# Optimization experiments

Hardware: AMD Instinct MI355X
Metric: run time of the kernel (lower is better)

Reference implementation:

```python
import jax, jax.numpy as jnp
import numpy as np
from jax import lax

B, T, IN_DIM, HID, K_WIN, N_TAGS, N_LAYERS = 128, 1024, 42, 256, 11, 8, 5
PAD = K_WIN // 2


def conv1d(x, w, b, pad):
    # x: (B, C_in, T), w: (C_out, C_in, K) -> (B, C_out, T)
    out = lax.conv_general_dilated(x, w, (1,), [(pad, pad)],
                                   dimension_numbers=('NCH', 'OIH', 'NCH'))
    return out + b[None, :, None]


def setup_inputs() -> dict:
    key = jax.random.key(0)
    ks = jax.random.split(key, 20)
    inp = {}
    inp['x'] = jax.random.normal(ks[0], (B, T, IN_DIM), dtype=jnp.float32)
    inp['lengths'] = jnp.full((B,), T, dtype=jnp.int32)
    inp['mask'] = jnp.ones((B, T), dtype=bool)
    inp['tags'] = jax.random.randint(ks[1], (B, T), 0, N_TAGS).astype(jnp.int32)
    prev = IN_DIM
    for i in range(N_LAYERS):
        scale = 1.0 / np.sqrt(prev * K_WIN)
        inp[f'w{i}'] = jax.random.uniform(ks[2 + i], (HID, prev, K_WIN), minval=-scale, maxval=scale, dtype=jnp.float32)
        inp[f'b{i}'] = jax.random.uniform(ks[8 + i], (HID,), minval=-scale, maxval=scale, dtype=jnp.float32)
        prev = HID
    scale = 1.0 / np.sqrt(HID)
    inp['w_out'] = jax.random.uniform(ks[14], (N_TAGS, HID, 1), minval=-scale, maxval=scale, dtype=jnp.float32)
    inp['b_out'] = jax.random.uniform(ks[15], (N_TAGS,), minval=-scale, maxval=scale, dtype=jnp.float32)
    # torchcrf initializes transitions uniform(-0.1, 0.1)
    inp['start_trans'] = jax.random.uniform(ks[16], (N_TAGS,), minval=-0.1, maxval=0.1, dtype=jnp.float32)
    inp['end_trans'] = jax.random.uniform(ks[17], (N_TAGS,), minval=-0.1, maxval=0.1, dtype=jnp.float32)
    inp['trans'] = jax.random.uniform(ks[18], (N_TAGS, N_TAGS), minval=-0.1, maxval=0.1, dtype=jnp.float32)
    return inp


def _emissions(x, ws, bs, w_out, b_out):
    h = jnp.transpose(x, (0, 2, 1))  # (B, C, T)
    for w, b in zip(ws, bs):
        h = jnp.tanh(conv1d(h, w, b, PAD))
    em = conv1d(h, w_out, b_out, 0)  # (B, K, T)
    return jnp.transpose(em, (0, 2, 1))  # (B, T, K)


def _crf_nll(emissions, tags, mask, start_trans, end_trans, trans):
    # loss = -sum_b log p(tags_b | emissions_b); torchcrf reduction='sum'
    Bn = emissions.shape[0]
    maskf = mask.astype(emissions.dtype)
    idx_b = jnp.arange(Bn)
    # --- numerator: path score of gold tags ---
    score0 = start_trans[tags[:, 0]] + emissions[idx_b, 0, tags[:, 0]]
    em_rest = jnp.transpose(emissions[:, 1:], (1, 0, 2))   # (T-1, B, K)
    tag_rest = tags[:, 1:].T                                # (T-1, B)
    m_rest = maskf[:, 1:].T                                 # (T-1, B)

    def num_step(carry, inp):
        score, prev_tag = carry
        em_t, tag_t, m_t = inp
        step = trans[prev_tag, tag_t] + em_t[idx_b, tag_t]
        score = score + step * m_t
        prev_tag = jnp.where(m_t > 0, tag_t, prev_tag)
        return (score, prev_tag), None

    (score, last_tag), _ = lax.scan(num_step, (score0, tags[:, 0]), (em_rest, tag_rest, m_rest))
    score = score + end_trans[last_tag]
    # --- denominator: forward algorithm (log partition) ---
    alpha0 = start_trans[None, :] + emissions[:, 0]  # (B, K)

    def den_step(alpha, inp):
        em_t, m_t = inp
        nxt = jax.nn.logsumexp(alpha[:, :, None] + trans[None, :, :] + em_t[:, None, :], axis=1)
        return jnp.where(m_t[:, None] > 0, nxt, alpha), None

    alpha, _ = lax.scan(den_step, alpha0, (em_rest, m_rest))
    log_z = jax.nn.logsumexp(alpha + end_trans[None, :], axis=1)
    return -jnp.sum(score - log_z)


def reference(x, lengths, mask, tags, w0, b0, w1, b1, w2, b2, w3, b3, w4, b4,
              w_out, b_out, start_trans, end_trans, trans):
    em = _emissions(x, [w0, w1, w2, w3, w4], [b0, b1, b2, b3, b4], w_out, b_out)
    return _crf_nll(em, tags, mask, start_trans, end_trans, trans)
```

## Files before the change

kernel.cpp:

```cpp
#include <hip/hip_runtime.h>


#define B_ 128
#define T_ 1024
#define IN_DIM_ 42
#define HID_ 256
#define KW_ 11
#define NTAGS_ 8
#define SEG_ 32
#define SEGL_ (T_ / SEG_)

typedef __bf16 bf16x8 __attribute__((ext_vector_type(8)));
typedef float f32x4 __attribute__((ext_vector_type(4)));
typedef short s16x8 __attribute__((ext_vector_type(8)));
typedef int i32x4 __attribute__((ext_vector_type(4)));
typedef int i32x8 __attribute__((ext_vector_type(8)));

struct i4pair { i32x4 lo, hi; };
__device__ __forceinline__ i32x8 mk8(i32x4 lo, i32x4 hi) {
    i4pair p{lo, hi};
    return __builtin_bit_cast(i32x8, p);
}

__device__ __forceinline__ unsigned short f2bf(float f) {
    unsigned u = __builtin_bit_cast(unsigned, f);
    u += 0x7FFFu + ((u >> 16) & 1u);
    return (unsigned short)(u >> 16);
}
__device__ __forceinline__ float fast_tanh(float x) {
    float e = __expf(2.f * x);
    return 1.f - 2.f / (e + 1.f);
}
__device__ __forceinline__ unsigned char f2fp8(float v) {
    return (unsigned char)(__builtin_amdgcn_cvt_pk_fp8_f32(v, v, 0, false) & 0xff);
}

#define SZ0_ (KW_ * 2 * 16 * 512)
#define SZF8_ (22 * 16 * 64 * 32)

__global__ void pack_l0(const float* __restrict__ w0, unsigned short* __restrict__ wp) {
    for (int idx = blockIdx.x * 256 + threadIdx.x; idx < SZ0_;
         idx += gridDim.x * 256) {
        int it2 = idx >> 13;
        int cic = it2 & 1, k = it2 >> 1;
        int e    = idx & 7;
        int lane = (idx >> 3) & 63;
        int coc  = (idx >> 9) & 15;
        int co = coc * 16 + (lane & 15);
        int ci = cic * 32 + ((lane >> 4) & 3) * 8 + e;
        float v = (ci < IN_DIM_) ? w0[(co * IN_DIM_ + ci) * KW_ + k] : 0.f;
        wp[idx] = f2bf(v);
    }
}

__global__ void pack_f8(const float* __restrict__ w1, const float* __restrict__ w2,
                        const float* __restrict__ w3, const float* __restrict__ w4,
                        unsigned char* __restrict__ wp8) {
    const int total = 4 * SZF8_;
    for (int idx = blockIdx.x * 256 + threadIdx.x; idx < total;
         idx += gridDim.x * 256) {
        int L   = idx / SZF8_;
        int loc = idx - L * SZF8_;
        const float* w = (L == 0) ? w1 : (L == 1) ? w2 : (L == 2) ? w3 : w4;
        int e    = loc & 31;
        int lane = (loc >> 5) & 63;
        int coc  = (loc >> 11) & 15;
        int it   = loc >> 15;
        int cic  = it / KW_;
        int k    = it - cic * KW_;
        int co = coc * 16 + (lane & 15);
        int ci = cic * 128 + (lane >> 4) * 32 + e;
        wp8[idx] = f2fp8(256.f * w[(co * HID_ + ci) * KW_ + k]);
    }
}

__global__ __launch_bounds__(512, 4)
void conv_first(const float* __restrict__ x, const unsigned short* __restrict__ wpack,
                const float* __restrict__ bias, unsigned char* __restrict__ out) {
    constexpr int CIN = 64, ROWS = 138;
    __shared__ unsigned short lds[ROWS * CIN];

    const int tid  = threadIdx.x;
    const int wave = tid >> 6;
    const int lane = tid & 63;
    const int l15  = lane & 15;
    const int lhi  = lane >> 4;
    const int wr   = wave >> 2;
    const int wc   = wave & 3;
    const int b    = blockIdx.x >> 3;
    const int t0   = (blockIdx.x & 7) * 128;

    for (int u = tid; u < ROWS * 32; u += 512) {
        int r = u >> 5, m = u & 31;
        int gt = t0 - 5 + r;
        unsigned val = 0;
        if (gt >= 0 && gt < T_ && 2 * m < IN_DIM_) {
            float2 f = *(const float2*)&x[((size_t)b * T_ + gt) * IN_DIM_ + 2 * m];
            val = (unsigned)f2bf(f.x) | ((unsigned)f2bf(f.y) << 16);
        }
        int c = m >> 2;
        int p = c ^ ((r + 3) & 7);
        ((unsigned*)lds)[(r * CIN + p * 8) / 2 + (m & 3)] = val;
    }
    __syncthreads();

    f32x4 acc[4][4];
#pragma unroll
    for (int tf = 0; tf < 4; ++tf)
#pragma unroll
        for (int n = 0; n < 4; ++n) acc[tf][n] = (f32x4){0.f, 0.f, 0.f, 0.f};

    const unsigned short* wpq = wpack + (size_t)(wc * 4) * 512 + lane * 8;
    const int arow = (wr * 64 + l15) * CIN;
    const int l153 = l15 + 3;

    s16x8 Bq[2][4];
#pragma unroll
    for (int n = 0; n < 4; ++n) Bq[0][n] = *(const s16x8*)&wpq[n * 512];

#pragma unroll
    for (int k = 0; k < KW_; ++k) {
#pragma unroll
        for (int cic = 0; cic < 2; ++cic) {
            const int it2 = k * 2 + cic;
            const int nxt = it2 + 1;
#pragma unroll
            for (int n = 0; n < 4; ++n)
                Bq[nxt & 1][n] = *(const s16x8*)&wpq[(size_t)nxt * 8192 + n * 512];
            const int key = (l153 + k) & 7;
            const int ao  = arow + (((cic * 4 + lhi) ^ key) << 3);
            s16x8 a0 = *(const s16x8*)&lds[ao + (0 * 16 + k) * CIN];
            s16x8 a1 = *(const s16x8*)&lds[ao + (1 * 16 + k) * CIN];
            s16x8 a2 = *(const s16x8*)&lds[ao + (2 * 16 + k) * CIN];
            s16x8 a3 = *(const s16x8*)&lds[ao + (3 * 16 + k) * CIN];
            __builtin_amdgcn_s_setprio(1);
#pragma unroll
            for (int n = 0; n < 4; ++n) {
                bf16x8 bb = __builtin_bit_cast(bf16x8, Bq[it2 & 1][n]);
                acc[0][n] = __builtin_amdgcn_mfma_f32_16x16x32_bf16(
                    __builtin_bit_cast(bf16x8, a0), bb, acc[0][n], 0, 0, 0);
                acc[1][n] = __builtin_amdgcn_mfma_f32_16x16x32_bf16(
                    __builtin_bit_cast(bf16x8, a1), bb, acc[1][n], 0, 0, 0);
                acc[2][n] = __builtin_amdgcn_mfma_f32_16x16x32_bf16(
                    __builtin_bit_cast(bf16x8, a2), bb, acc[2][n], 0, 0, 0);
                acc[3][n] = __builtin_amdgcn_mfma_f32_16x16x32_bf16(
                    __builtin_bit_cast(bf16x8, a3), bb, acc[3][n], 0, 0, 0);
            }
            __builtin_amdgcn_s_setprio(0);
        }
    }

#pragma unroll
    for (int n = 0; n < 4; ++n) {
        int co = wc * 64 + n * 16 + l15;
        float bv = bias[co];
        int cch = co >> 4, cby = co & 15;
#pragma unroll
        for (int tf = 0; tf < 4; ++tf) {
#pragma unroll
            for (int r4 = 0; r4 < 4; ++r4) {
                int t = t0 + wr * 64 + tf * 16 + lhi * 4 + r4;
                float v = fast_tanh(acc[tf][n][r4] + bv);
                out[((size_t)b * T_ + t) * 256 + ((cch ^ (t & 15)) << 4) + cby] =
                    f2fp8(v);
            }
        }
    }
}

template <bool LAST>
__global__ __launch_bounds__(256, 3)
void conv_mid(const unsigned char* __restrict__ Hin,
              const unsigned char* __restrict__ wpack,
              const float* __restrict__ bias, unsigned char* __restrict__ out,
              const float* __restrict__ w_out, float* __restrict__ emout) {
    extern __shared__ unsigned char lds8[];

    const int tid  = threadIdx.x;
    const int wave = tid >> 6;
    const int lane = tid & 63;
    const int l15  = lane & 15;
    const int lhi  = lane >> 4;
    const int wc   = wave;
    const int b    = blockIdx.x >> 4;
    const int t0   = (blockIdx.x & 15) * 64;

    for (int c = wave; c < 19; c += 4) {
        int r0 = c * 4;
        int r  = r0 + (lane >> 4);
        int gt = t0 - 5 + r;
        gt = gt < 0 ? 0 : (gt >= T_ ? T_ - 1 : gt);
        const unsigned char* src =
            Hin + ((size_t)b * T_ + gt) * 256 + (lane & 15) * 16;
        __builtin_amdgcn_global_load_lds(
            (const __attribute__((address_space(1))) void*)src,
            (__attribute__((address_space(3))) void*)&lds8[r0 * 256], 16, 0, 0);
    }
    __syncthreads();
    if (t0 == 0) {
        for (int u = tid; u < 320; u += 256)
            ((unsigned*)lds8)[u] = 0;
    }
    if (t0 == T_ - 64) {
        for (int u = tid; u < 320; u += 256)
            ((unsigned*)&lds8[69 * 256])[u] = 0;
    }
    __syncthreads();

    f32x4 acc[4][4];
#pragma unroll
    for (int tf = 0; tf < 4; ++tf)
#pragma unroll
        for (int n = 0; n < 4; ++n) acc[tf][n] = (f32x4){0.f, 0.f, 0.f, 0.f};

    const unsigned char* wpB = wpack + (size_t)(wc * 4) * 2048 + lane * 32;

    i32x8 Aa[4], Bq[4];

#define LOAD_B(n_, itv)                                                        \
    {                                                                          \
        const unsigned char* p_ = wpB + (size_t)(itv) * 32768 + (n_) * 2048;   \
        Bq[n_] = mk8(*(const i32x4*)p_, *(const i32x4*)(p_ + 16));             \
    }

#pragma unroll
    for (int n = 0; n < 4; ++n) LOAD_B(n, 0);

#pragma unroll 1
    for (int kk = 0; kk < 22; ++kk) {
        const int cic_ = kk / KW_;
        const int kn_  = kk - cic_ * KW_;
        const int key_ = (l15 + kn_ + 11) & 15;
        const int ca_  = ((cic_ * 8 + lhi * 2) ^ key_) << 4;
        const int rb_  = (l15 + kn_) * 256 + ca_;
#pragma unroll
        for (int tf = 0; tf < 4; ++tf)
            Aa[tf] = mk8(*(const i32x4*)&lds8[rb_ + tf * 4096],
                         *(const i32x4*)&lds8[(rb_ + tf * 4096) ^ 16]);
#pragma unroll
        for (int n = 0; n < 4; ++n) {
            __builtin_amdgcn_s_setprio(1);
#pragma unroll
            for (int tf = 0; tf < 4; ++tf)
                acc[tf][n] = __builtin_amdgcn_mfma_scale_f32_16x16x128_f8f6f4(
                    Aa[tf], Bq[n], acc[tf][n], 0, 0,
                    0, 0x7F7F7F7F, 0, 0x7F7F7F7F);
            __builtin_amdgcn_s_setprio(0);
            LOAD_B(n, kk + 1);
        }
    }
#undef LOAD_B

    constexpr float INV = 1.f / 256.f;
    if constexpr (!LAST) {
#pragma unroll
        for (int n = 0; n < 4; ++n) {
            int co = wc * 64 + n * 16 + l15;
            float bv = bias[co];
            int cch = co >> 4, cby = co & 15;
#pragma unroll
            for (int tf = 0; tf < 4; ++tf) {
#pragma unroll
                for (int r4 = 0; r4 < 4; ++r4) {
                    int t = t0 + tf * 16 + lhi * 4 + r4;
                    float v = fast_tanh(acc[tf][n][r4] * INV + bv);
                    out[((size_t)b * T_ + t) * 256 + ((cch ^ (t & 15)) << 4) + cby] =
                        f2fp8(v);
                }
            }
        }
    } else {
        float wv[4][NTAGS_], bvn[4];
#pragma unroll
        for (int n = 0; n < 4; ++n) {
            int co = wc * 64 + n * 16 + l15;
            bvn[n] = bias[co];
#pragma unroll
            for (int tg = 0; tg < NTAGS_; ++tg) wv[n][tg] = w_out[tg * HID_ + co];
        }
        __syncthreads();
        float* pbuf = (float*)lds8;
#pragma unroll
        for (int tf = 0; tf < 4; ++tf) {
#pragma unroll
            for (int r4 = 0; r4 < 4; ++r4) {
                float h[4];
#pragma unroll
                for (int n = 0; n < 4; ++n)
                    h[n] = fast_tanh(acc[tf][n][r4] * INV + bvn[n]);
                float pt[NTAGS_];
#pragma unroll
                for (int tg = 0; tg < NTAGS_; ++tg)
                    pt[tg] = h[0] * wv[0][tg] + h[1] * wv[1][tg] +
                             h[2] * wv[2][tg] + h[3] * wv[3][tg];
#pragma unroll
                for (int off = 8; off; off >>= 1)
#pragma unroll
                    for (int tg = 0; tg < NTAGS_; ++tg)
                        pt[tg] += __shfl_down(pt[tg], off);
                if (l15 == 0) {
                    int tloc = tf * 16 + lhi * 4 + r4;
                    f32x4 lo = {pt[0], pt[1], pt[2], pt[3]};
                    f32x4 hi = {pt[4], pt[5], pt[6], pt[7]};
                    *(f32x4*)&pbuf[(wc * 64 + tloc) * 8]     = lo;
                    *(f32x4*)&pbuf[(wc * 64 + tloc) * 8 + 4] = hi;
                }
            }
        }
        __syncthreads();
        for (int u = tid; u < 64 * NTAGS_; u += 256) {
            float s = pbuf[u] + pbuf[512 + u] + pbuf[1024 + u] + pbuf[1536 + u];
            emout[((size_t)b * T_ + t0) * NTAGS_ + u] = s;
        }
    }
}

__global__ __launch_bounds__(256)
void crf_seg_kernel(const float* __restrict__ em, const float* __restrict__ tr,
                    const float* __restrict__ bo, float* __restrict__ segM) {
    const int gw   = blockIdx.x * 4 + (threadIdx.x >> 6);
    const int b    = gw >> 5;
    const int s    = gw & 31;
    const int lane = threadIdx.x & 63;
    const int i    = lane >> 3;
    const int j    = lane & 7;
    const float* emb = em + (size_t)b * T_ * NTAGS_;
    const float boj = bo[j];

    float tc[8];
#pragma unroll
    for (int k = 0; k < 8; ++k) tc[k] = tr[k * 8 + j];

    const int tb = (s == 0) ? 1 : s * SEGL_;
    const int te = (s + 1) * SEGL_;

    float m = tr[i * 8 + j] + emb[tb * 8 + j] + boj;
    for (int t = tb + 1; t < te; ++t) {
        float emt = emb[t * 8 + j] + boj;
        float v[8];
#pragma unroll
        for (int k = 0; k < 8; ++k) v[k] = __shfl(m, (lane & 56) + k) + tc[k];
        float mx = fmaxf(fmaxf(fmaxf(v[0], v[1]), fmaxf(v[2], v[3])),
                         fmaxf(fmaxf(v[4], v[5]), fmaxf(v[6], v[7])));
        float sm = 0.f;
#pragma unroll
        for (int k = 0; k < 8; ++k) sm += __expf(v[k] - mx);
        m = mx + __logf(sm) + emt;
    }
    segM[(size_t)gw * 64 + lane] = m;
}

__global__ __launch_bounds__(64)
void crf_kernel(const float* __restrict__ em, const float* __restrict__ segM,
                const int* __restrict__ tags,
                const float* __restrict__ st, const float* __restrict__ et,
                const float* __restrict__ tr, const float* __restrict__ bo,
                float* __restrict__ outp) {
    __shared__ float sM[SEG_ * 64];
    const int b    = blockIdx.x;
    const int lane = threadIdx.x;
    const float* emb = em + (size_t)b * T_ * NTAGS_;
    const int*   tg  = tags + (size_t)b * T_;

    for (int u = lane; u < SEG_ * 64; u += 64)
        sM[u] = segM[(size_t)b * SEG_ * 64 + u];

    const float breg = bo[lane & 7];

    float num = 0.f;
    for (int t = 1 + lane; t < T_; t += 64) {
        int pt = tg[t - 1], ct = tg[t];
        num += tr[pt * NTAGS_ + ct] + emb[t * NTAGS_ + ct] + __shfl(breg, ct);
    }
#pragma unroll
    for (int off = 32; off; off >>= 1) num += __shfl_down(num, off);
    int tgf = tg[0], tgl = tg[T_ - 1];
    float bo_f = __shfl(breg, tgf);
    float score = 0.f;
    if (lane == 0)
        score = num + st[tgf] + emb[tgf] + bo_f + et[tgl];

    __syncthreads();

    const int j = lane & 7;
    float alpha = st[j] + emb[j] + breg;
    for (int sgm = 0; sgm < SEG_; ++sgm) {
        const float* M = &sM[sgm * 64];
        float v[8];
#pragma unroll
        for (int i = 0; i < 8; ++i) v[i] = __shfl(alpha, i) + M[i * 8 + j];
        float mx = fmaxf(fmaxf(fmaxf(v[0], v[1]), fmaxf(v[2], v[3])),
                         fmaxf(fmaxf(v[4], v[5]), fmaxf(v[6], v[7])));
        float sm = 0.f;
#pragma unroll
        for (int i = 0; i < 8; ++i) sm += __expf(v[i] - mx);
        alpha = mx + __logf(sm);
    }
    float vj = alpha + et[j];
    float w[8];
#pragma unroll
    for (int i = 0; i < 8; ++i) w[i] = __shfl(vj, i);
    float m2 = w[0];
#pragma unroll
    for (int i = 1; i < 8; ++i) m2 = fmaxf(m2, w[i]);
    float s2 = 0.f;
#pragma unroll
    for (int i = 0; i < 8; ++i) s2 += __expf(w[i] - m2);
    float log_z = m2 + __logf(s2);

    if (lane == 0) atomicAdd(outp, log_z - score);
}

extern "C" void kernel_launch(void* const* d_in, const int* in_sizes, int n_in,
                              void* d_out, int out_size, void* d_ws, size_t ws_size,
                              hipStream_t stream) {
    const float* x     = (const float*)d_in[0];
    const int*   tags  = (const int*)d_in[3];
    const float* w[5]  = {(const float*)d_in[4], (const float*)d_in[6],
                          (const float*)d_in[8], (const float*)d_in[10],
                          (const float*)d_in[12]};
    const float* bias[5] = {(const float*)d_in[5], (const float*)d_in[7],
                            (const float*)d_in[9], (const float*)d_in[11],
                            (const float*)d_in[13]};
    const float* w_out = (const float*)d_in[14];
    const float* b_out = (const float*)d_in[15];
    const float* st    = (const float*)d_in[16];
    const float* et    = (const float*)d_in[17];
    const float* tr    = (const float*)d_in[18];

    unsigned char* H0 = (unsigned char*)d_ws;
    unsigned char* H1 = H0 + (size_t)B_ * T_ * 256;
    unsigned short* wp0 = (unsigned short*)(H1 + (size_t)B_ * T_ * 256);
    unsigned char* wpf8 = (unsigned char*)(wp0 + SZ0_);
    float* em   = (float*)(wpf8 + 4 * (size_t)SZF8_);
    float* segM = em + (size_t)B_ * T_ * NTAGS_;

    pack_l0<<<176, 256, 0, stream>>>(w[0], wp0);
    pack_f8<<<2048, 256, 0, stream>>>(w[1], w[2], w[3], w[4], wpf8);

    conv_first<<<B_ * (T_ / 128), 512, 0, stream>>>(x, wp0, bias[0], H0);

    const int NBLK = B_ * (T_ / 64);
    const int MLDS = 76 * 256;
    unsigned char* wpl[4] = {wpf8, wpf8 + SZF8_, wpf8 + 2 * (size_t)SZF8_,
                             wpf8 + 3 * (size_t)SZF8_};
    conv_mid<false><<<NBLK, 256, MLDS, stream>>>(H0, wpl[0], bias[1], H1,
                                                 nullptr, nullptr);
    conv_mid<false><<<NBLK, 256, MLDS, stream>>>(H1, wpl[1], bias[2], H0,
                                                 nullptr, nullptr);
    conv_mid<false><<<NBLK, 256, MLDS, stream>>>(H0, wpl[2], bias[3], H1,
                                                 nullptr, nullptr);
    conv_mid<true><<<NBLK, 256, MLDS, stream>>>(H1, wpl[3], bias[4], nullptr,
                                                w_out, em);

    crf_seg_kernel<<<B_ * SEG_ / 4, 256, 0, stream>>>(em, tr, b_out, segM);

    hipMemsetAsync(d_out, 0, sizeof(float), stream);
    crf_kernel<<<B_, 64, 0, stream>>>(em, segM, tags, st, et, tr, b_out,
                                      (float*)d_out);
}
```

Measured before the change: 477.5 us.

## Cut B-fragment registers to two slots and raise conv_mid occupancy to 4

The weight-fragment prefetch in conv_mid now cycles through two register slots instead of four, loading the next fragment right after each MFMA group consumes one. This frees VGPRs so the launch bound can ask for 4 blocks per CU instead of 3, giving more waves to hide latency. The cost is a shorter prefetch distance for the global weight loads, since each load has only one MFMA group to cover its latency before use. The tighter register budget also risks spilling.

```diff
diff --git a/kernel.cpp b/kernel.cpp
--- a/kernel.cpp
+++ b/kernel.cpp
@@ -169,7 +169,7 @@
 }
 
 template <bool LAST>
-__global__ __launch_bounds__(256, 3)
+__global__ __launch_bounds__(256, 4)
 void conv_mid(const unsigned char* __restrict__ Hin,
               const unsigned char* __restrict__ wpack,
               const float* __restrict__ bias, unsigned char* __restrict__ out,
@@ -215,16 +215,25 @@
 
     const unsigned char* wpB = wpack + (size_t)(wc * 4) * 2048 + lane * 32;
 
-    i32x8 Aa[4], Bq[4];
-
-#define LOAD_B(n_, itv)                                                        \
+    i32x8 Aa[4], Bs0, Bs1;
+
+#define LOAD_BS(SLOT, itv, nv)                                                 \
     {                                                                          \
-        const unsigned char* p_ = wpB + (size_t)(itv) * 32768 + (n_) * 2048;   \
-        Bq[n_] = mk8(*(const i32x4*)p_, *(const i32x4*)(p_ + 16));             \
-    }
-
-#pragma unroll
-    for (int n = 0; n < 4; ++n) LOAD_B(n, 0);
+        const unsigned char* p_ = wpB + (size_t)(itv) * 32768 + (nv) * 2048;   \
+        SLOT = mk8(*(const i32x4*)p_, *(const i32x4*)(p_ + 16));               \
+    }
+#define CL(BS, n_)                                                             \
+    {                                                                          \
+        __builtin_amdgcn_s_setprio(1);                                         \
+        _Pragma("unroll") for (int tf = 0; tf < 4; ++tf)                       \
+            acc[tf][n_] = __builtin_amdgcn_mfma_scale_f32_16x16x128_f8f6f4(    \
+                Aa[tf], BS, acc[tf][n_], 0, 0,                                 \
+                0, 0x7F7F7F7F, 0, 0x7F7F7F7F);               \
+        __builtin_amdgcn_s_setprio(0);                                         \
+    }
+
+    LOAD_BS(Bs0, 0, 0);
+    LOAD_BS(Bs1, 0, 1);
 
 #pragma unroll 1
     for (int kk = 0; kk < 22; ++kk) {
@@ -237,19 +246,13 @@
         for (int tf = 0; tf < 4; ++tf)
             Aa[tf] = mk8(*(const i32x4*)&lds8[rb_ + tf * 4096],
                          *(const i32x4*)&lds8[(rb_ + tf * 4096) ^ 16]);
-#pragma unroll
-        for (int n = 0; n < 4; ++n) {
-            __builtin_amdgcn_s_setprio(1);
-#pragma unroll
-            for (int tf = 0; tf < 4; ++tf)
-                acc[tf][n] = __builtin_amdgcn_mfma_scale_f32_16x16x128_f8f6f4(
-                    Aa[tf], Bq[n], acc[tf][n], 0, 0,
-                    0, 0x7F7F7F7F, 0, 0x7F7F7F7F);
-            __builtin_amdgcn_s_setprio(0);
-            LOAD_B(n, kk + 1);
-        }
-    }
-#undef LOAD_B
+        CL(Bs0, 0); LOAD_BS(Bs0, kk, 2);
+        CL(Bs1, 1); LOAD_BS(Bs1, kk, 3);
+        CL(Bs0, 2); LOAD_BS(Bs0, kk + 1, 0);
+        CL(Bs1, 3); LOAD_BS(Bs1, kk + 1, 1);
+    }
+#undef LOAD_BS
+#undef CL
 
     constexpr float INV = 1.f / 256.f;
     if constexpr (!LAST) {
```

After: 477.0 us. About the same (-0.1%).
